# Kernel optimization log

Hardware: AMD Instinct MI355X
Metric: run time of the kernel (lower is better)

Reference implementation:

```python
import jax, jax.numpy as jnp
import numpy as np

IDIM = 128
C = 3
NB_SAMPLES = 128
R = 32768
SH_C0 = 0.28209479177387814
SH_C1 = 0.4886025119029199
SH_C2 = np.array([1.0925484305920792, -1.0925484305920792, 0.31539156525252005,
                  -1.0925484305920792, 0.5462742152960396], dtype=np.float32)


def eval_sh_bases(d):
    # d: (R,3) unit directions -> (R,9) degree-2 real SH basis
    x, y, z = d[:, 0], d[:, 1], d[:, 2]
    return jnp.stack([
        jnp.full_like(x, SH_C0),
        -SH_C1 * y, SH_C1 * z, -SH_C1 * x,
        SH_C2[0] * x * y, SH_C2[1] * y * z,
        SH_C2[2] * (2.0 * z * z - x * x - y * y),
        SH_C2[3] * x * z, SH_C2[4] * (x * x - y * y)], axis=-1)


def trilerp(pts, grid):
    # pts: (N,3) in voxel coords (box_min=0, delta_voxel=1); grid: (D,D,D,F)
    D = grid.shape[0]
    p = jnp.clip(pts, 0.0, D - 1 - 1e-4)
    i0 = jnp.floor(p).astype(jnp.int32)
    w = p - i0.astype(p.dtype)          # (N,3) fractional weights
    i1 = jnp.minimum(i0 + 1, D - 1)
    out = jnp.zeros((pts.shape[0], grid.shape[-1]), dtype=p.dtype)
    for dx in (0, 1):
        wx = w[:, 0] if dx else 1.0 - w[:, 0]
        ix = i1[:, 0] if dx else i0[:, 0]
        for dy in (0, 1):
            wy = w[:, 1] if dy else 1.0 - w[:, 1]
            iy = i1[:, 1] if dy else i0[:, 1]
            for dz in (0, 1):
                wz = w[:, 2] if dz else 1.0 - w[:, 2]
                iz = i1[:, 2] if dz else i0[:, 2]
                out = out + (wx * wy * wz)[:, None] * grid[ix, iy, iz]
    return out


def setup_inputs() -> dict:
    key = jax.random.key(0)
    k = jax.random.split(key, 6)
    x = jax.random.uniform(k[0], (R, 3), jnp.float32) * (IDIM - 1)
    d = jax.random.normal(k[1], (R, 3), jnp.float32)
    d = d / jnp.linalg.norm(d, axis=1, keepdims=True)
    tmin = jax.random.uniform(k[2], (R,), jnp.float32) * 5.0
    tmax = tmin + 20.0 + jax.random.uniform(k[3], (R,), jnp.float32) * 80.0
    grid = jax.random.uniform(k[4], (IDIM, IDIM, IDIM, 9 * C), jnp.float32)
    opacity = jax.random.uniform(k[5], (IDIM, IDIM, IDIM, 1), jnp.float32)
    return {"x": x, "d": d, "tmin": tmin, "tmax": tmax, "grid": grid, "opacity": opacity}


def reference(x, d, tmin, tmax, grid, opacity):
    nb_rays = x.shape[0]
    # samples = arange(0.05, 0.95, 1/nb_samples): S entries
    S = int(np.floor(0.9 * NB_SAMPLES - 1e-6)) + 1
    base = 0.05 + jnp.arange(S, dtype=x.dtype) / NB_SAMPLES            # (S,)
    samples = (tmax - tmin)[:, None] * base[None, :] + tmin[:, None]   # (R,S)
    pts = x[:, None, :] + samples[..., None] * d[:, None, :]           # (R,S,3)
    sh = eval_sh_bases(d)                                              # (R,9)
    flat = pts.reshape(-1, 3)
    coeffs = trilerp(flat, grid).reshape(nb_rays, S, C, 9)             # (R,S,C,9)
    op = jnp.clip(trilerp(flat, opacity), 0.0, 100000.0).reshape(nb_rays, S)
    harm = coeffs * sh[:, None, None, :]                               # (R,S,C,9)
    samples_color = jnp.clip(harm.sum(axis=3) + 0.5, 0.0, 100000.0)    # (R,S,C)
    deltas = samples[:, 1:] - samples[:, :-1]                          # (R,S-1)
    dts = -(deltas * op[:, :-1])
    cum = jnp.concatenate([jnp.zeros((nb_rays, 1), dtype=x.dtype),
                           jnp.cumsum(dts, axis=1)[:, :-1]], axis=1)
    w = jnp.exp(cum) * (1.0 - jnp.exp(dts))                            # (R,S-1)
    rays_color = jnp.sum(w[..., None] * samples_color[:, :-1, :], axis=1)  # (R,C)
    return rays_color
```

## Files before the change

### kernel.cpp

```cpp
#include <hip/hip_runtime.h>

#define NS 115
#define WEPS 5e-5f
#define LOG_TSKIP -6.9078f

typedef float f32x4 __attribute__((ext_vector_type(4)));
typedef float f32x2 __attribute__((ext_vector_type(2)));

struct SH9 { float a,b,c,d,e,f,g,h,i; };

__device__ __forceinline__ f32x4 load4(const float* p) {
    f32x4 v;
    __builtin_memcpy(&v, p, 16);
    return v;
}
__device__ __forceinline__ f32x2 load2(const float* p) {
    f32x2 v;
    __builtin_memcpy(&v, p, 8);
    return v;
}

__device__ __forceinline__ void pos_to_cell(float px, float py, float pz,
                                            int& ibase, float* wxs, float* wys, float* wzs) {
    px = fminf(fmaxf(px, 0.0f), 126.9999f);
    py = fminf(fmaxf(py, 0.0f), 126.9999f);
    pz = fminf(fmaxf(pz, 0.0f), 126.9999f);
    int ix = (int)px, iy = (int)py, iz = (int)pz;
    float wx = px - (float)ix, wy = py - (float)iy, wz = pz - (float)iz;
    ibase = (ix << 14) + (iy << 7) + iz;
    wxs[0] = 1.0f - wx; wxs[1] = wx;
    wys[0] = 1.0f - wy; wys[1] = wy;
    wzs[0] = 1.0f - wz; wzs[1] = wz;
}

__device__ __forceinline__ float eval_op(float px, float py, float pz,
                                         const float* __restrict__ opa) {
    int ibase; float wxs[2], wys[2], wzs[2];
    pos_to_cell(px, py, pz, ibase, wxs, wys, wzs);
    float op = 0.0f;
    #pragma unroll
    for (int cx = 0; cx < 2; ++cx)
    #pragma unroll
    for (int cy = 0; cy < 2; ++cy) {
        int idx = ibase + (cx << 14) + (cy << 7);
        f32x2 pr = load2(opa + idx);
        float wxy = wxs[cx] * wys[cy];
        op = fmaf(wxy * wzs[0], pr.x, op);
        op = fmaf(wxy * wzs[1], pr.y, op);
    }
    return fminf(fmaxf(op, 0.0f), 100000.0f);
}

__device__ __forceinline__ void eval_color(float px, float py, float pz,
                                           const float* __restrict__ grid,
                                           const SH9& sh,
                                           float& cr, float& cg, float& cb) {
    int ibase; float wxs[2], wys[2], wzs[2];
    pos_to_cell(px, py, pz, ibase, wxs, wys, wzs);
    float r = 0.0f, g = 0.0f, b = 0.0f;
    #pragma unroll
    for (int cx = 0; cx < 2; ++cx)
    #pragma unroll
    for (int cy = 0; cy < 2; ++cy)
    #pragma unroll
    for (int cz = 0; cz < 2; ++cz) {
        int idx = ibase + (cx << 14) + (cy << 7) + cz;
        float wc = wxs[cx] * wys[cy] * wzs[cz];
        const float* cp = grid + (size_t)idx * 27;
        f32x4 v0 = load4(cp);
        f32x4 v1 = load4(cp + 4);
        f32x4 v2 = load4(cp + 8);
        f32x4 v3 = load4(cp + 12);
        f32x4 v4 = load4(cp + 16);
        f32x4 v5 = load4(cp + 20);
        f32x4 v6 = load4(cp + 23);
        float c0 = sh.a*v0.x + sh.b*v0.y + sh.c*v0.z + sh.d*v0.w
                 + sh.e*v1.x + sh.f*v1.y + sh.g*v1.z + sh.h*v1.w + sh.i*v2.x;
        float c1 = sh.a*v2.y + sh.b*v2.z + sh.c*v2.w + sh.d*v3.x
                 + sh.e*v3.y + sh.f*v3.z + sh.g*v3.w + sh.h*v4.x + sh.i*v4.y;
        float c2 = sh.a*v4.z + sh.b*v4.w + sh.c*v5.x + sh.d*v5.y
                 + sh.e*v5.z + sh.f*v5.w + sh.g*v6.y + sh.h*v6.z + sh.i*v6.w;
        r = fmaf(wc, c0, r);
        g = fmaf(wc, c1, g);
        b = fmaf(wc, c2, b);
    }
    cr = fminf(fmaxf(r + 0.5f, 0.0f), 100000.0f);
    cg = fminf(fmaxf(g + 0.5f, 0.0f), 100000.0f);
    cb = fminf(fmaxf(b + 0.5f, 0.0f), 100000.0f);
}

__device__ __forceinline__ float wave_incl_scan(float v, int lane) {
    #pragma unroll
    for (int off = 1; off < 64; off <<= 1) {
        float n = __shfl_up(v, (unsigned)off, 64);
        if (lane >= off) v += n;
    }
    return v;
}

__global__ __launch_bounds__(256) void rf_kernel(
    const float* __restrict__ x, const float* __restrict__ d,
    const float* __restrict__ tmin, const float* __restrict__ tmax,
    const float* __restrict__ grid, const float* __restrict__ opa,
    float* __restrict__ out, int nrays)
{
    int gtid = blockIdx.x * blockDim.x + threadIdx.x;
    int ray = __builtin_amdgcn_readfirstlane(gtid >> 6);
    int lane = threadIdx.x & 63;
    if (ray >= nrays) return;

    float ox = x[3*ray+0], oy = x[3*ray+1], oz = x[3*ray+2];
    float ddx = d[3*ray+0], ddy = d[3*ray+1], ddz = d[3*ray+2];
    float t0 = tmin[ray], t1 = tmax[ray];
    float range = t1 - t0;
    float delta = range * 0.0078125f;

    SH9 sh;
    sh.a = 0.28209479177387814f;
    sh.b = -0.4886025119029199f * ddy;
    sh.c =  0.4886025119029199f * ddz;
    sh.d = -0.4886025119029199f * ddx;
    sh.e =  1.0925484305920792f * ddx * ddy;
    sh.f = -1.0925484305920792f * ddy * ddz;
    sh.g =  0.31539156525252005f * (2.0f*ddz*ddz - ddx*ddx - ddy*ddy);
    sh.h = -1.0925484305920792f * ddx * ddz;
    sh.i =  0.5462742152960396f * (ddx*ddx - ddy*ddy);

    float accR = 0.0f, accG = 0.0f, accB = 0.0f;

    {
        int s = lane;
        float t = range * (0.05f + (float)s * 0.0078125f) + t0;
        float px = ox + t*ddx, py = oy + t*ddy, pz = oz + t*ddz;
        float opv = eval_op(px, py, pz, opa);
        float dts = -delta * opv;
        float incl = wave_incl_scan(dts, lane);
        float cum = incl - dts;
        float total0 = __shfl(incl, 63, 64);
        float w = __expf(cum) * (1.0f - __expf(dts));
        if (w > WEPS) {
            float cr, cg, cb;
            eval_color(px, py, pz, grid, sh, cr, cg, cb);
            accR = w * cr; accG = w * cg; accB = w * cb;
        }
        if (total0 > LOG_TSKIP) {
            int s1 = 64 + lane;
            float dts1 = 0.0f;
            float px1 = 0.f, py1 = 0.f, pz1 = 0.f;
            if (s1 < NS) {
                float t1s = range * (0.05f + (float)s1 * 0.0078125f) + t0;
                px1 = ox + t1s*ddx; py1 = oy + t1s*ddy; pz1 = oz + t1s*ddz;
                float opv1 = eval_op(px1, py1, pz1, opa);
                dts1 = -delta * opv1;
            }
            float incl1 = wave_incl_scan(dts1, lane);
            float cum1 = total0 + incl1 - dts1;
            float w1 = __expf(cum1) * (1.0f - __expf(dts1));
            if (w1 > WEPS) {
                float cr, cg, cb;
                eval_color(px1, py1, pz1, grid, sh, cr, cg, cb);
                accR = fmaf(w1, cr, accR);
                accG = fmaf(w1, cg, accG);
                accB = fmaf(w1, cb, accB);
            }
        }
    }

    #pragma unroll
    for (int off = 32; off > 0; off >>= 1) {
        accR += __shfl_xor(accR, off, 64);
        accG += __shfl_xor(accG, off, 64);
        accB += __shfl_xor(accB, off, 64);
    }
    if (lane == 0) {
        out[3*ray+0] = accR;
        out[3*ray+1] = accG;
        out[3*ray+2] = accB;
    }
}

extern "C" void kernel_launch(void* const* d_in, const int* in_sizes, int n_in,
                              void* d_out, int out_size, void* d_ws, size_t ws_size,
                              hipStream_t stream) {
    const float* x    = (const float*)d_in[0];
    const float* d    = (const float*)d_in[1];
    const float* tmin = (const float*)d_in[2];
    const float* tmax = (const float*)d_in[3];
    const float* grid = (const float*)d_in[4];
    const float* opa  = (const float*)d_in[5];
    float* out = (float*)d_out;

    int nrays = in_sizes[0] / 3;
    int threads = 256;
    int blocks = (nrays * 64 + threads - 1) / threads;
    rf_kernel<<<blocks, threads, 0, stream>>>(x, d, tmin, tmax, grid, opa, out, nrays);
}
```

Measured before the change: 434.0 us.

## Repack SH grid to padded fp16 layout in workspace before rendering

Adds a pre-pass kernel that converts the 27-float-per-cell SH coefficient grid into a 32-half (64-byte) aligned fp16 layout in the workspace. The render kernel then reads each trilinear corner with three 16-byte loads and one 8-byte load instead of seven unaligned float4 loads, which halves the bytes gathered and aligns corners to cache lines. The cost is a full pass over the roughly 226 MB grid on every call plus fp16 rounding of the coefficients. If the workspace is too small it falls back to the fp32 path.

```diff
diff --git a/kernel.cpp b/kernel.cpp
--- a/kernel.cpp
+++ b/kernel.cpp
@@ -3,22 +3,20 @@
 #define NS 115
 #define WEPS 5e-5f
 #define LOG_TSKIP -6.9078f
+#define NCELLS (128*128*128)
+#define PACK_BYTES ((size_t)NCELLS * 64)
 
 typedef float f32x4 __attribute__((ext_vector_type(4)));
 typedef float f32x2 __attribute__((ext_vector_type(2)));
+typedef _Float16 h16x8 __attribute__((ext_vector_type(8)));
+typedef _Float16 h16x4 __attribute__((ext_vector_type(4)));
 
 struct SH9 { float a,b,c,d,e,f,g,h,i; };
 
-__device__ __forceinline__ f32x4 load4(const float* p) {
-    f32x4 v;
-    __builtin_memcpy(&v, p, 16);
-    return v;
-}
-__device__ __forceinline__ f32x2 load2(const float* p) {
-    f32x2 v;
-    __builtin_memcpy(&v, p, 8);
-    return v;
-}
+__device__ __forceinline__ f32x4 load4(const float* p) { f32x4 v; __builtin_memcpy(&v, p, 16); return v; }
+__device__ __forceinline__ f32x2 load2(const float* p) { f32x2 v; __builtin_memcpy(&v, p, 8);  return v; }
+__device__ __forceinline__ h16x8 load8h(const _Float16* p) { h16x8 v; __builtin_memcpy(&v, p, 16); return v; }
+__device__ __forceinline__ h16x4 load4h(const _Float16* p) { h16x4 v; __builtin_memcpy(&v, p, 8);  return v; }
 
 __device__ __forceinline__ void pos_to_cell(float px, float py, float pz,
                                             int& ibase, float* wxs, float* wys, float* wzs) {
@@ -51,10 +49,48 @@
     return fminf(fmaxf(op, 0.0f), 100000.0f);
 }
 
-__device__ __forceinline__ void eval_color(float px, float py, float pz,
-                                           const float* __restrict__ grid,
-                                           const SH9& sh,
-                                           float& cr, float& cg, float& cb) {
+__device__ __forceinline__ void eval_color_h(float px, float py, float pz,
+                                             const _Float16* __restrict__ pack,
+                                             const SH9& sh,
+                                             float& cr, float& cg, float& cb) {
+    int ibase; float wxs[2], wys[2], wzs[2];
+    pos_to_cell(px, py, pz, ibase, wxs, wys, wzs);
+    float r = 0.0f, g = 0.0f, b = 0.0f;
+    #pragma unroll
+    for (int cx = 0; cx < 2; ++cx)
+    #pragma unroll
+    for (int cy = 0; cy < 2; ++cy)
+    #pragma unroll
+    for (int cz = 0; cz < 2; ++cz) {
+        int idx = ibase + (cx << 14) + (cy << 7) + cz;
+        float wc = wxs[cx] * wys[cy] * wzs[cz];
+        const _Float16* cp = pack + ((size_t)idx << 5);
+        h16x8 v0 = load8h(cp);
+        h16x8 v1 = load8h(cp + 8);
+        h16x8 v2 = load8h(cp + 16);
+        h16x4 v3 = load4h(cp + 24);
+        float c0 = sh.a*(float)v0[0] + sh.b*(float)v0[1] + sh.c*(float)v0[2] + sh.d*(float)v0[3]
+                 + sh.e*(float)v0[4] + sh.f*(float)v0[5] + sh.g*(float)v0[6] + sh.h*(float)v0[7]
+                 + sh.i*(float)v1[0];
+        float c1 = sh.a*(float)v1[1] + sh.b*(float)v1[2] + sh.c*(float)v1[3] + sh.d*(float)v1[4]
+                 + sh.e*(float)v1[5] + sh.f*(float)v1[6] + sh.g*(float)v1[7] + sh.h*(float)v2[0]
+                 + sh.i*(float)v2[1];
+        float c2 = sh.a*(float)v2[2] + sh.b*(float)v2[3] + sh.c*(float)v2[4] + sh.d*(float)v2[5]
+                 + sh.e*(float)v2[6] + sh.f*(float)v2[7] + sh.g*(float)v3[0] + sh.h*(float)v3[1]
+                 + sh.i*(float)v3[2];
+        r = fmaf(wc, c0, r);
+        g = fmaf(wc, c1, g);
+        b = fmaf(wc, c2, b);
+    }
+    cr = fminf(fmaxf(r + 0.5f, 0.0f), 100000.0f);
+    cg = fminf(fmaxf(g + 0.5f, 0.0f), 100000.0f);
+    cb = fminf(fmaxf(b + 0.5f, 0.0f), 100000.0f);
+}
+
+__device__ __forceinline__ void eval_color_f(float px, float py, float pz,
+                                             const float* __restrict__ grid,
+                                             const SH9& sh,
+                                             float& cr, float& cg, float& cb) {
     int ibase; float wxs[2], wys[2], wzs[2];
     pos_to_cell(px, py, pz, ibase, wxs, wys, wzs);
     float r = 0.0f, g = 0.0f, b = 0.0f;
@@ -98,10 +134,41 @@
     return v;
 }
 
+__global__ __launch_bounds__(256) void pack_kernel(const float* __restrict__ grid,
+                                                   _Float16* __restrict__ pack) {
+    int cell = blockIdx.x * blockDim.x + threadIdx.x;
+    if (cell >= NCELLS) return;
+    const float* src = grid + (size_t)cell * 27;
+    float t[28];
+    f32x4 a0 = load4(src);      f32x4 a1 = load4(src + 4);
+    f32x4 a2 = load4(src + 8);  f32x4 a3 = load4(src + 12);
+    f32x4 a4 = load4(src + 16); f32x4 a5 = load4(src + 20);
+    t[0]=a0.x;t[1]=a0.y;t[2]=a0.z;t[3]=a0.w;
+    t[4]=a1.x;t[5]=a1.y;t[6]=a1.z;t[7]=a1.w;
+    t[8]=a2.x;t[9]=a2.y;t[10]=a2.z;t[11]=a2.w;
+    t[12]=a3.x;t[13]=a3.y;t[14]=a3.z;t[15]=a3.w;
+    t[16]=a4.x;t[17]=a4.y;t[18]=a4.z;t[19]=a4.w;
+    t[20]=a5.x;t[21]=a5.y;t[22]=a5.z;t[23]=a5.w;
+    t[24]=src[24];t[25]=src[25];t[26]=src[26];t[27]=0.0f;
+    h16x8 o0, o1, o2;
+    h16x4 o3;
+    #pragma unroll
+    for (int i = 0; i < 8; ++i) { o0[i]=(_Float16)t[i]; o1[i]=(_Float16)t[8+i]; o2[i]=(_Float16)t[16+i]; }
+    #pragma unroll
+    for (int i = 0; i < 4; ++i) o3[i]=(_Float16)t[24+i];
+    _Float16* dst = pack + ((size_t)cell << 5);
+    __builtin_memcpy(dst,      &o0, 16);
+    __builtin_memcpy(dst + 8,  &o1, 16);
+    __builtin_memcpy(dst + 16, &o2, 16);
+    __builtin_memcpy(dst + 24, &o3, 8);
+}
+
+template <bool PACKED>
 __global__ __launch_bounds__(256) void rf_kernel(
     const float* __restrict__ x, const float* __restrict__ d,
     const float* __restrict__ tmin, const float* __restrict__ tmax,
-    const float* __restrict__ grid, const float* __restrict__ opa,
+    const float* __restrict__ grid, const _Float16* __restrict__ pack,
+    const float* __restrict__ opa,
     float* __restrict__ out, int nrays)
 {
     int gtid = blockIdx.x * blockDim.x + threadIdx.x;
@@ -140,7 +207,8 @@
         float w = __expf(cum) * (1.0f - __expf(dts));
         if (w > WEPS) {
             float cr, cg, cb;
-            eval_color(px, py, pz, grid, sh, cr, cg, cb);
+            if (PACKED) eval_color_h(px, py, pz, pack, sh, cr, cg, cb);
+            else        eval_color_f(px, py, pz, grid, sh, cr, cg, cb);
             accR = w * cr; accG = w * cg; accB = w * cb;
         }
         if (total0 > LOG_TSKIP) {
@@ -158,7 +226,8 @@
             float w1 = __expf(cum1) * (1.0f - __expf(dts1));
             if (w1 > WEPS) {
                 float cr, cg, cb;
-                eval_color(px1, py1, pz1, grid, sh, cr, cg, cb);
+                if (PACKED) eval_color_h(px1, py1, pz1, pack, sh, cr, cg, cb);
+                else        eval_color_f(px1, py1, pz1, grid, sh, cr, cg, cb);
                 accR = fmaf(w1, cr, accR);
                 accG = fmaf(w1, cg, accG);
                 accB = fmaf(w1, cb, accB);
@@ -193,5 +262,12 @@
     int nrays = in_sizes[0] / 3;
     int threads = 256;
     int blocks = (nrays * 64 + threads - 1) / threads;
-    rf_kernel<<<blocks, threads, 0, stream>>>(x, d, tmin, tmax, grid, opa, out, nrays);
-}
+
+    if (ws_size >= PACK_BYTES) {
+        _Float16* pack = (_Float16*)d_ws;
+        pack_kernel<<<(NCELLS + 255) / 256, 256, 0, stream>>>(grid, pack);
+        rf_kernel<true><<<blocks, threads, 0, stream>>>(x, d, tmin, tmax, grid, pack, opa, out, nrays);
+    } else {
+        rf_kernel<false><<<blocks, threads, 0, stream>>>(x, d, tmin, tmax, grid, nullptr, opa, out, nrays);
+    }
+}
```

After: 447.6 us. +3.1%, slower.
